# Kernel tuning notes

Measured on AMD Instinct MI355X. Metric: run time of the kernel, lower is better.

Reference implementation:

```python
import jax, jax.numpy as jnp
import numpy as np
from jax import lax

B, CIN, COUT, K, H, W = 32, 64, 64, 3, 160, 160
STRIDE, PAD = 1, 1


def setup_inputs() -> dict:
    key = jax.random.key(0)
    kx, kw = jax.random.split(key)
    x = jax.random.normal(kx, (B, CIN, H, W), dtype=jnp.float32)
    # xavier_normal-ish init for the full-precision weight [Cout, Cin, K, K]
    fan_in, fan_out = CIN * K * K, COUT * K * K
    std = float(np.sqrt(2.0 / (fan_in + fan_out)))
    w = jax.random.normal(kw, (COUT, CIN, K, K), dtype=jnp.float32) * std
    return {"x": x, "w": w}


def reference(x, w):
    # Binarize activations: sign (bi_act_method=0)
    xb = jnp.sign(x)
    # Weight path (bi_w_scale=2): clamp to [-1,1], per-output-channel |w| mean scale
    wc = jnp.clip(w, -1.0, 1.0)
    mean_val = jnp.mean(jnp.abs(wc), axis=(1, 2, 3), keepdims=True)  # [Cout,1,1,1]
    bw = jnp.sign(wc) * mean_val
    # conv2d, NCHW / OIHW
    out = lax.conv_general_dilated(
        xb, bw,
        window_strides=(STRIDE, STRIDE),
        padding=((PAD, PAD), (PAD, PAD)),
        dimension_numbers=("NCHW", "OIHW", "NCHW"),
    )
    return out
```

## Files before the change

kernel.cpp:

```cpp
#include <hip/hip_runtime.h>
#include <cstdint>

#define WID   160
#define HEI   160
#define HWPIX (WID * HEI)
#define CIN_  64
#define COUT_ 64
#define BATCH 32
#define PW    162
#define PPIX  (PW * PW)
#define NBORDER 636

__global__ __launch_bounds__(64) void wprep_kernel(const float* __restrict__ w,
                                                   uint64_t* __restrict__ wpack,
                                                   float* __restrict__ alpha) {
    const int co = blockIdx.x;
    const int ci = threadIdx.x;
    const float* wp = w + ((size_t)co * CIN_ + ci) * 9;

    float vals[9];
    float s = 0.0f;
#pragma unroll
    for (int t = 0; t < 9; ++t) {
        float v = wp[t];
        vals[t] = v;
        s += fminf(fabsf(v), 1.0f);
    }
#pragma unroll
    for (int t = 0; t < 9; ++t) {
        unsigned long long m = __ballot(vals[t] > 0.0f);
        if (ci == 0) wpack[co * 9 + t] = m;
    }
#pragma unroll
    for (int off = 32; off > 0; off >>= 1) s += __shfl_down(s, off);
    if (ci == 0) alpha[co] = s * (1.0f / 576.0f);
}

__global__ __launch_bounds__(256) void binpack_kernel(const float* __restrict__ x,
                                                      uint64_t* __restrict__ packed) {
    const int t  = blockIdx.x * 256 + threadIdx.x;
    const int b  = blockIdx.y;
    const int p4 = t * 4;
    const int y  = p4 / WID;
    const int x0 = p4 - y * WID;
    const float4* xp = (const float4*)(x + (size_t)b * CIN_ * HWPIX + p4);

    uint32_t lo[4] = {0, 0, 0, 0}, hi[4] = {0, 0, 0, 0};
#pragma unroll
    for (int ci = 0; ci < 32; ++ci) {
        float4 v = xp[(size_t)ci * (HWPIX / 4)];
        lo[0] |= (uint32_t)(v.x > 0.0f) << ci;
        lo[1] |= (uint32_t)(v.y > 0.0f) << ci;
        lo[2] |= (uint32_t)(v.z > 0.0f) << ci;
        lo[3] |= (uint32_t)(v.w > 0.0f) << ci;
    }
#pragma unroll
    for (int ci = 0; ci < 32; ++ci) {
        float4 v = xp[(size_t)(ci + 32) * (HWPIX / 4)];
        hi[0] |= (uint32_t)(v.x > 0.0f) << ci;
        hi[1] |= (uint32_t)(v.y > 0.0f) << ci;
        hi[2] |= (uint32_t)(v.z > 0.0f) << ci;
        hi[3] |= (uint32_t)(v.w > 0.0f) << ci;
    }
    uint64_t* dst = packed + (size_t)b * PPIX + (size_t)(y + 1) * PW + (x0 + 1);
#pragma unroll
    for (int i = 0; i < 4; ++i)
        dst[i] = ((uint64_t)hi[i] << 32) | lo[i];
}

__global__ __launch_bounds__(256) void conv_kernel(const uint64_t* __restrict__ packed,
                                                   const uint64_t* __restrict__ wpack,
                                                   const float* __restrict__ alpha,
                                                   float* __restrict__ out) {
    const int pix = blockIdx.x * 256 + threadIdx.x;
    const int b   = blockIdx.y;
    const int y   = pix / WID;
    const int x   = pix - y * WID;
    const uint64_t* pb = packed + (size_t)b * PPIX + (size_t)y * PW + x;

    uint64_t p[9];
#pragma unroll
    for (int ky = 0; ky < 3; ++ky)
#pragma unroll
        for (int kx = 0; kx < 3; ++kx)
            p[ky * 3 + kx] = pb[(size_t)ky * PW + kx];

    float* op = out + (size_t)b * COUT_ * HWPIX + pix;
#pragma unroll 4
    for (int co = 0; co < COUT_; ++co) {
        int pc = 0;
#pragma unroll
        for (int t = 0; t < 9; ++t)
            pc += __popcll(p[t] ^ wpack[co * 9 + t]);
        const float a = alpha[co];
        op[(size_t)co * HWPIX] = fmaf((float)pc, -2.0f * a, 576.0f * a);
    }
}

__global__ __launch_bounds__(256) void fixup_kernel(const uint64_t* __restrict__ packed,
                                                    const uint64_t* __restrict__ wpack,
                                                    const float* __restrict__ alpha,
                                                    float* __restrict__ out) {
    const int t = blockIdx.x * 256 + threadIdx.x;
    if (t >= NBORDER * BATCH) return;
    const int b = t / NBORDER;
    const int i = t - b * NBORDER;
    int x, y;
    if      (i < 160) { y = 0;       x = i;       }
    else if (i < 320) { y = 159;     x = i - 160; }
    else if (i < 478) { x = 0;       y = i - 319; }
    else              { x = 159;     y = i - 477; }

    const uint64_t* pb = packed + (size_t)b * PPIX + (size_t)y * PW + x;
    uint64_t p[9];
    int valid[9];
    int nv = 0;
#pragma unroll
    for (int ky = 0; ky < 3; ++ky)
#pragma unroll
        for (int kx = 0; kx < 3; ++kx) {
            const int yy = y + ky - 1, xx = x + kx - 1;
            const int v = (yy >= 0) && (yy < HEI) && (xx >= 0) && (xx < WID);
            valid[ky * 3 + kx] = v;
            nv += v;
            p[ky * 3 + kx] = pb[(size_t)ky * PW + kx];
        }
    float* op = out + (size_t)b * COUT_ * HWPIX + (size_t)y * WID + x;
    for (int co = 0; co < COUT_; ++co) {
        int pc = 0;
#pragma unroll
        for (int tt = 0; tt < 9; ++tt)
            pc += valid[tt] ? __popcll(p[tt] ^ wpack[co * 9 + tt]) : 0;
        op[(size_t)co * HWPIX] = alpha[co] * (float)((nv << 6) - 2 * pc);
    }
}

extern "C" void kernel_launch(void* const* d_in, const int* in_sizes, int n_in,
                              void* d_out, int out_size, void* d_ws, size_t ws_size,
                              hipStream_t stream) {
    const float* x = (const float*)d_in[0];
    const float* w = (const float*)d_in[1];
    float* out = (float*)d_out;

    uint64_t* wpack  = (uint64_t*)d_ws;
    float*    alpha  = (float*)((char*)d_ws + 4608);
    uint64_t* packed = (uint64_t*)((char*)d_ws + 8192);

    hipMemsetAsync(packed, 0, (size_t)BATCH * PPIX * sizeof(uint64_t), stream);

    wprep_kernel<<<dim3(COUT_), dim3(64), 0, stream>>>(w, wpack, alpha);
    binpack_kernel<<<dim3(HWPIX / 4 / 256, BATCH), dim3(256), 0, stream>>>(x, packed);
    conv_kernel<<<dim3(HWPIX / 256, BATCH), dim3(256), 0, stream>>>(packed, wpack, alpha, out);
    fixup_kernel<<<dim3((NBORDER * BATCH + 255) / 256), dim3(256), 0, stream>>>(packed, wpack, alpha, out);
}
```

Baseline: 446.9 us.

## Compute four adjacent pixels per thread and split output channels across grid z

Each conv thread now produces four horizontally adjacent output pixels. It loads a 3x6 window of packed words once and reuses each weight word across the four pixels. Output channels are split into two halves along grid z, and results are written as float4 vector stores. This cuts redundant packed-input loads and weight reads per output and widens the stores, but it raises register pressure and lowers the thread count per batch image.

```diff
diff --git a/kernel.cpp b/kernel.cpp
--- a/kernel.cpp
+++ b/kernel.cpp
@@ -72,28 +72,51 @@
                                                    const uint64_t* __restrict__ wpack,
                                                    const float* __restrict__ alpha,
                                                    float* __restrict__ out) {
-    const int pix = blockIdx.x * 256 + threadIdx.x;
+    const int g   = blockIdx.x * 256 + threadIdx.x;
     const int b   = blockIdx.y;
-    const int y   = pix / WID;
-    const int x   = pix - y * WID;
-    const uint64_t* pb = packed + (size_t)b * PPIX + (size_t)y * PW + x;
+    const int coh = blockIdx.z;
+    const int p4  = g * 4;
+    const int y   = p4 / WID;
+    const int x0  = p4 - y * WID;
+    const uint64_t* pb = packed + (size_t)b * PPIX + (size_t)y * PW + x0;
 
-    uint64_t p[9];
+    uint64_t t[18];
 #pragma unroll
-    for (int ky = 0; ky < 3; ++ky)
+    for (int r = 0; r < 3; ++r)
 #pragma unroll
-        for (int kx = 0; kx < 3; ++kx)
-            p[ky * 3 + kx] = pb[(size_t)ky * PW + kx];
+        for (int c = 0; c < 6; ++c)
+            t[r * 6 + c] = pb[(size_t)r * PW + c];
 
-    float* op = out + (size_t)b * COUT_ * HWPIX + pix;
-#pragma unroll 4
-    for (int co = 0; co < COUT_; ++co) {
-        int pc = 0;
+    float* op = out + ((size_t)b * COUT_ + (size_t)coh * 32) * HWPIX + p4;
+
+#pragma unroll 2
+    for (int ci = 0; ci < 32; ++ci) {
+        const int co = coh * 32 + ci;
+        const uint64_t* wkp = wpack + co * 9;
+        uint64_t wk[9];
 #pragma unroll
-        for (int t = 0; t < 9; ++t)
-            pc += __popcll(p[t] ^ wpack[co * 9 + t]);
-        const float a = alpha[co];
-        op[(size_t)co * HWPIX] = fmaf((float)pc, -2.0f * a, 576.0f * a);
+        for (int k = 0; k < 9; ++k) wk[k] = wkp[k];
+
+        int pc0 = 0, pc1 = 0, pc2 = 0, pc3 = 0;
+#pragma unroll
+        for (int r = 0; r < 3; ++r)
+#pragma unroll
+            for (int c = 0; c < 3; ++c) {
+                const uint64_t wv = wk[r * 3 + c];
+                pc0 += __popcll(t[r * 6 + c + 0] ^ wv);
+                pc1 += __popcll(t[r * 6 + c + 1] ^ wv);
+                pc2 += __popcll(t[r * 6 + c + 2] ^ wv);
+                pc3 += __popcll(t[r * 6 + c + 3] ^ wv);
+            }
+        const float a  = alpha[co];
+        const float m  = -2.0f * a;
+        const float c5 = 576.0f * a;
+        float4 res;
+        res.x = fmaf((float)pc0, m, c5);
+        res.y = fmaf((float)pc1, m, c5);
+        res.z = fmaf((float)pc2, m, c5);
+        res.w = fmaf((float)pc3, m, c5);
+        *(float4*)(op + (size_t)ci * HWPIX) = res;
     }
 }
 
@@ -150,6 +173,6 @@
 
     wprep_kernel<<<dim3(COUT_), dim3(64), 0, stream>>>(w, wpack, alpha);
     binpack_kernel<<<dim3(HWPIX / 4 / 256, BATCH), dim3(256), 0, stream>>>(x, packed);
-    conv_kernel<<<dim3(HWPIX / 256, BATCH), dim3(256), 0, stream>>>(packed, wpack, alpha, out);
+    conv_kernel<<<dim3(HWPIX / 4 / 256, BATCH, 2), dim3(256), 0, stream>>>(packed, wpack, alpha, out);
     fixup_kernel<<<dim3((NBORDER * BATCH + 255) / 256), dim3(256), 0, stream>>>(packed, wpack, alpha, out);
 }
```

After: 450.6 us. About the same (+0.8%).
